# Optimization experiments

Hardware: AMD Instinct MI355X
Metric: run time of the kernel (lower is better)

The kernel has to match this reference:

```python
import jax, jax.numpy as jnp
import numpy as np

N_EMBD = 2048
HEAD_DIM = 128
N_CTX = 2048
BATCH = 8
SEQ = 2048


def setup_inputs() -> dict:
    key = jax.random.key(0)
    ks = jax.random.split(key, 7)
    s = 1.0 / np.sqrt(N_EMBD)
    x = jax.random.normal(ks[0], (BATCH, SEQ, N_EMBD), dtype=jnp.float32)
    # torch Linear params: weight (out, in), bias (out,)
    Wq = jax.random.uniform(ks[1], (HEAD_DIM, N_EMBD), jnp.float32, -s, s)
    bq = jax.random.uniform(ks[2], (HEAD_DIM,), jnp.float32, -s, s)
    Wk = jax.random.uniform(ks[3], (HEAD_DIM, N_EMBD), jnp.float32, -s, s)
    bk = jax.random.uniform(ks[4], (HEAD_DIM,), jnp.float32, -s, s)
    Wv = jax.random.uniform(ks[5], (HEAD_DIM, N_EMBD), jnp.float32, -s, s)
    bv = jax.random.uniform(ks[6], (HEAD_DIM,), jnp.float32, -s, s)
    return {"x": x, "Wq": Wq, "bq": bq, "Wk": Wk, "bk": bk, "Wv": Wv, "bv": bv}


def reference(x, Wq, bq, Wk, bk, Wv, bv):
    # projections: y = x @ W^T + b
    q = jnp.einsum('bse,de->bsd', x, Wq) + bq  # (B, S, D)
    k = jnp.einsum('bse,de->bsd', x, Wk) + bk
    v = jnp.einsum('bse,de->bsd', x, Wv) + bv
    seq = x.shape[1]
    scores = jnp.einsum('bqd,bkd->bqk', q, k)  # (B, S, S)
    # causal mask: strictly-upper-triangular positions set to -inf (before scaling, as in source)
    causal = jnp.triu(jnp.ones((seq, seq), dtype=bool), k=1)
    scores = jnp.where(causal[None, :, :], -jnp.inf, scores)
    # NOTE: source scales by sqrt(seq_size), not sqrt(head_dim)
    weight = jax.nn.softmax(scores / jnp.sqrt(jnp.float32(seq)), axis=-1)
    return jnp.einsum('bqk,bkd->bqd', weight, v)
```

## Files before the change

kernel.cpp:

```cpp
#include <hip/hip_runtime.h>
#include <cmath>

#define BATCH 8
#define SEQ   2048
#define NEMB  2048
#define HD    128
#define NROWS (BATCH * SEQ)

typedef __bf16 v8bf __attribute__((ext_vector_type(8)));
typedef float  f32x4 __attribute__((ext_vector_type(4)));

union U8 { v8bf v; __bf16 b[8]; unsigned short e[8]; };
union F4 { f32x4 v; float f[4]; };

__device__ inline void async16(void* lds, const void* g) {
  __builtin_amdgcn_global_load_lds(
      (const __attribute__((address_space(1))) unsigned int*)g,
      (__attribute__((address_space(3))) unsigned int*)lds, 16, 0, 0);
}

__device__ inline v8bf cvt8(float4 a, float4 b) {
  U8 u;
  u.b[0] = (__bf16)a.x; u.b[1] = (__bf16)a.y; u.b[2] = (__bf16)a.z; u.b[3] = (__bf16)a.w;
  u.b[4] = (__bf16)b.x; u.b[5] = (__bf16)b.y; u.b[6] = (__bf16)b.z; u.b[7] = (__bf16)b.w;
  return u.v;
}

__global__ __launch_bounds__(256) void wpack_kernel(
    const float* __restrict__ Wq, const float* __restrict__ Wk,
    const float* __restrict__ Wv, __bf16* __restrict__ out) {
  const int idx = blockIdx.x * 256 + threadIdx.x;
  const int lane = idx & 63;
  const int g = idx >> 6;
  const int fg = g & 7;
  const int tt = (g >> 3) & 31;
  const int wn = (g >> 8) & 1;
  const int p  = g >> 9;
  const int n = fg >> 1, kk = fg & 1;
  const int row = wn * 64 + n * 16 + (lane & 15);
  const int k   = tt * 64 + kk * 32 + (lane >> 4) * 8;
  const float* __restrict__ W = p == 0 ? Wq : p == 1 ? Wk : Wv;
  const float4* s = (const float4*)(W + (size_t)row * NEMB + k);
  float4 f0 = s[0], f1 = s[1];
  *(v8bf*)(out + (size_t)idx * 8) = cvt8(f0, f1);
}

__global__ __launch_bounds__(256, 3) void qkv_proj_kernel(
    const float* __restrict__ x, const __bf16* __restrict__ Wpack,
    const float* __restrict__ bq, const float* __restrict__ bk,
    const float* __restrict__ bv,
    __bf16* __restrict__ Qb, __bf16* __restrict__ Kb, __bf16* __restrict__ Vb)
{
  const int bid0 = blockIdx.x;
  const int bid = ((bid0 & 7) * 96) + (bid0 >> 3);
  const int mt = bid / 3;
  const int proj = bid % 3;
  const float* __restrict__ bias = proj == 0 ? bq : proj == 1 ? bk : bv;
  __bf16* __restrict__ Out = proj == 0 ? Qb : proj == 1 ? Kb : Vb;
  const int m0 = mt * 64;

  __shared__ float Asm[64 * 64];

  const int t = threadIdx.x, lane = t & 63, w = t >> 6;
  const int wm = w >> 1, wn = w & 1;
  const int hi = lane >> 4, lo = lane & 15;

  const float* pa[4];
  char* la[4];
#pragma unroll
  for (int i = 0; i < 4; ++i) {
    const int r = (w * 4 + i) * 4 + (lane >> 4);
    const int c = (lane & 15) ^ (r & 7);
    pa[i] = x + (size_t)(m0 + r) * NEMB + c * 4;
    la[i] = (char*)Asm + (w * 4 + i) * 1024;
  }

  const __bf16* bp = Wpack + (size_t)(proj * 2 + wn) * 131072 + lane * 8;

  f32x4 acc[2][4];
  const f32x4 fz = {0.f, 0.f, 0.f, 0.f};
#pragma unroll
  for (int m = 0; m < 2; ++m)
#pragma unroll
    for (int n = 0; n < 4; ++n) acc[m][n] = fz;

  v8bf B0[4][2], B1[4][2];
  auto LOADB = [&](v8bf (&B)[4][2], int tt) {
    const __bf16* p = bp + tt * 4096;
#pragma unroll
    for (int n = 0; n < 4; ++n)
#pragma unroll
      for (int kk = 0; kk < 2; ++kk)
        B[n][kk] = *(const v8bf*)(p + (n * 2 + kk) * 512);
  };
  auto STAGE_A = [&](int tt) {
    const int k0 = tt * 64;
#pragma unroll
    for (int i = 0; i < 4; ++i) async16(la[i], pa[i] + k0);
  };
  auto STEP = [&](v8bf (&B)[4][2]) {
#pragma unroll
    for (int kk = 0; kk < 2; ++kk) {
      v8bf a[2];
#pragma unroll
      for (int m = 0; m < 2; ++m) {
        const int r = wm * 32 + m * 16 + lo;
        const int s = kk * 8 + hi * 2;
        const char* rowp = (const char*)Asm + r * 256;
        F4 a0, a1;
        a0.v = *(const f32x4*)(rowp + (((s)     ^ (r & 7)) << 4));
        a1.v = *(const f32x4*)(rowp + (((s + 1) ^ (r & 7)) << 4));
        U8 u;
#pragma unroll
        for (int q = 0; q < 4; ++q) {
          u.b[q]     = (__bf16)a0.f[q];
          u.b[q + 4] = (__bf16)a1.f[q];
        }
        a[m] = u.v;
      }
#pragma unroll
      for (int m = 0; m < 2; ++m)
#pragma unroll
        for (int n = 0; n < 4; ++n)
          acc[m][n] = __builtin_amdgcn_mfma_f32_16x16x32_bf16(a[m], B[n][kk], acc[m][n], 0, 0, 0);
    }
  };

  const int NT = NEMB / 64;
  LOADB(B0, 0);
  for (int tt = 0; tt < NT; tt += 2) {
    __syncthreads();
    STAGE_A(tt);
    LOADB(B1, tt + 1);
    __syncthreads();
    STEP(B0);
    __syncthreads();
    STAGE_A(tt + 1);
    if (tt + 2 < NT) LOADB(B0, tt + 2);
    __syncthreads();
    STEP(B1);
  }

#pragma unroll
  for (int n = 0; n < 4; ++n) {
    const int col = wn * 64 + n * 16 + lo;
    const float bi = bias[col];
#pragma unroll
    for (int m = 0; m < 2; ++m) {
#pragma unroll
      for (int r = 0; r < 4; ++r) {
        const int row = m0 + wm * 32 + m * 16 + hi * 4 + r;
        Out[(size_t)row * HD + col] = (__bf16)(acc[m][n][r] + bi);
      }
    }
  }
}

__global__ __launch_bounds__(256) void attn_kernel(
    const __bf16* __restrict__ Qb, const __bf16* __restrict__ Kb,
    const __bf16* __restrict__ Vb, float* __restrict__ Opart,
    float* __restrict__ Ml)
{
  const int bid0 = blockIdx.x;
  const int bid = ((bid0 & 7) << 6) + (bid0 >> 3);
  const int b = bid >> 6;
  const int qs = bid & 63;
  const int qt = qs >> 1;
  const int s  = qs & 1;
  const int q0 = qt * 64;
  const int half = (qt + 2) >> 1;
  const int kv_beg = s ? half : 0;
  const int kv_end = s ? (qt + 1) : half;
  const int nst = kv_end - kv_beg;

  const int t = threadIdx.x, lane = t & 63, w = t >> 6;
  const int hi = lane >> 4, lo = lane & 15;

  __shared__ __bf16 Ksm[2][64 * 128];
  __shared__ __bf16 Vtsm[2][128 * 64];
  __shared__ __bf16 Psm[4][16 * 64];

  v8bf aQ[4];
  {
    const __bf16* qp = Qb + ((size_t)(b * SEQ + q0 + w * 16 + lo)) * HD + hi * 8;
#pragma unroll
    for (int kk = 0; kk < 4; ++kk) aQ[kk] = *(const v8bf*)(qp + kk * 32);
  }

  const __bf16* kga[4];
#pragma unroll
  for (int i = 0; i < 4; ++i) {
    const int r = (w * 4 + i) * 4 + (lane >> 4);
    const int c = (lane & 15) ^ (r & 7);
    kga[i] = Kb + ((size_t)(b * SEQ) + r) * HD + c * 8;
  }

  const int keyg = t >> 4, dg = t & 15;
  U8 vv[4];

  f32x4 accO[8];
  const f32x4 fz = {0.f, 0.f, 0.f, 0.f};
#pragma unroll
  for (int n = 0; n < 8; ++n) accO[n] = fz;
  float m_s[4], l_s[4];
#pragma unroll
  for (int r = 0; r < 4; ++r) { m_s[r] = -INFINITY; l_s[r] = 0.f; }

  const float scale = 0.022097086912079608f;

  if (nst > 0) {
    auto STAGE_K = [&](int kv, int buf) {
      const size_t off = (size_t)kv * 64 * HD;
      char* kb = (char*)&Ksm[buf][0];
#pragma unroll
      for (int i = 0; i < 4; ++i) async16(kb + (w * 4 + i) * 1024, kga[i] + off);
    };
    auto LOAD_V = [&](int kv) {
      const __bf16* vp = Vb + ((size_t)(b * SEQ + kv * 64 + keyg * 4)) * HD + dg * 8;
#pragma unroll
      for (int j = 0; j < 4; ++j) vv[j].v = *(const v8bf*)(vp + (size_t)j * HD);
    };
    auto WRITE_VT = [&](int buf) {
      char* vb2 = (char*)&Vtsm[buf][0];
#pragma unroll
      for (int dd = 0; dd < 8; ++dd) {
        const int d = (dd + dg) & 7;
        ushort4 pk = make_ushort4(vv[0].e[d], vv[1].e[d], vv[2].e[d], vv[3].e[d]);
        const int row = dg * 8 + d;
        *(ushort4*)(vb2 + row * 128 + ((keyg * 8) ^ ((row & 7) << 4))) = pk;
      }
    };

    STAGE_K(kv_beg, 0);
    LOAD_V(kv_beg);
    WRITE_VT(0);
    __syncthreads();

    for (int t2 = 0; t2 < nst; ++t2) {
      const int kv = kv_beg + t2;
      const int cur = t2 & 1;
      const bool more = (t2 + 1 < nst);
      if (more) { STAGE_K(kv + 1, cur ^ 1); LOAD_V(kv + 1); }

      f32x4 accS[4];
#pragma unroll
      for (int n = 0; n < 4; ++n) accS[n] = fz;
      const char* ksm = (const char*)&Ksm[cur][0];
#pragma unroll
      for (int kk = 0; kk < 4; ++kk) {
        const int cb = kk * 64 + hi * 16;
        v8bf bk[4];
#pragma unroll
        for (int n = 0; n < 4; ++n) {
          const int r = n * 16 + lo;
          bk[n] = *(const v8bf*)(ksm + r * 256 + (cb ^ ((r & 7) << 4)));
        }
#pragma unroll
        for (int n = 0; n < 4; ++n)
          accS[n] = __builtin_amdgcn_mfma_f32_16x16x32_bf16(aQ[kk], bk[n], accS[n], 0, 0, 0);
      }

      float sv[4][4];
      const bool diag = (kv == qt);
#pragma unroll
      for (int n = 0; n < 4; ++n)
#pragma unroll
        for (int r = 0; r < 4; ++r) {
          float v = accS[n][r] * scale;
          if (diag) {
            const int key = kv * 64 + n * 16 + lo;
            const int qr = q0 + w * 16 + hi * 4 + r;
            if (key > qr) v = -INFINITY;
          }
          sv[n][r] = v;
        }

      float mx[4];
#pragma unroll
      for (int r = 0; r < 4; ++r) {
        mx[r] = fmaxf(fmaxf(sv[0][r], sv[1][r]), fmaxf(sv[2][r], sv[3][r]));
#pragma unroll
        for (int off = 1; off < 16; off <<= 1)
          mx[r] = fmaxf(mx[r], __shfl_xor(mx[r], off));
      }
      float corr[4], p[4][4], rs[4];
#pragma unroll
      for (int r = 0; r < 4; ++r) {
        const float mnew = fmaxf(m_s[r], mx[r]);
        corr[r] = __expf(m_s[r] - mnew);
        m_s[r] = mnew;
        rs[r] = 0.f;
      }
#pragma unroll
      for (int n = 0; n < 4; ++n)
#pragma unroll
        for (int r = 0; r < 4; ++r) {
          p[n][r] = __expf(sv[n][r] - m_s[r]);
          rs[r] += p[n][r];
        }
#pragma unroll
      for (int r = 0; r < 4; ++r) {
#pragma unroll
        for (int off = 1; off < 16; off <<= 1) rs[r] += __shfl_xor(rs[r], off);
        l_s[r] = l_s[r] * corr[r] + rs[r];
      }
#pragma unroll
      for (int n = 0; n < 8; ++n)
#pragma unroll
        for (int r = 0; r < 4; ++r) accO[n][r] *= corr[r];

#pragma unroll
      for (int n = 0; n < 4; ++n)
#pragma unroll
        for (int r = 0; r < 4; ++r) {
          const int row = hi * 4 + r;
          __bf16 h = (__bf16)p[n][r];
          *(unsigned short*)((char*)&Psm[w][0] + row * 128 +
                             (((n * 16 + lo) * 2) ^ ((row & 7) << 4))) =
              __builtin_bit_cast(unsigned short, h);
        }

      if (more) WRITE_VT(cur ^ 1);

      const char* vsm = (const char*)&Vtsm[cur][0];
#pragma unroll
      for (int k2 = 0; k2 < 2; ++k2) {
        const int cb = k2 * 64 + hi * 16;
        const v8bf aP = *(const v8bf*)((const char*)&Psm[w][0] + lo * 128 + (cb ^ ((lo & 7) << 4)));
#pragma unroll
        for (int n = 0; n < 8; ++n) {
          const int r = n * 16 + lo;
          const v8bf bv = *(const v8bf*)(vsm + r * 128 + (cb ^ ((r & 7) << 4)));
          accO[n] = __builtin_amdgcn_mfma_f32_16x16x32_bf16(aP, bv, accO[n], 0, 0, 0);
        }
      }
      if (more) __syncthreads();
    }
  }

#pragma unroll
  for (int r = 0; r < 4; ++r) {
    const int qr = q0 + w * 16 + hi * 4 + r;
    float* op = Opart + ((size_t)s * NROWS + b * SEQ + qr) * HD + lo;
#pragma unroll
    for (int n = 0; n < 8; ++n) op[n * 16] = accO[n][r];
    if (lo == 0) {
      float* mlp = Ml + ((size_t)s * NROWS + b * SEQ + qr) * 2;
      mlp[0] = m_s[r];
      mlp[1] = l_s[r];
    }
  }
}

__global__ __launch_bounds__(256) void combine_kernel(
    const float* __restrict__ Opart, const float* __restrict__ Ml,
    float* __restrict__ out)
{
  const int idx = blockIdx.x * 256 + threadIdx.x;
  const int row = idx >> 1, h = idx & 1;
  const float m0 = Ml[(size_t)row * 2],           l0 = Ml[(size_t)row * 2 + 1];
  const float m1 = Ml[((size_t)NROWS + row) * 2], l1 = Ml[((size_t)NROWS + row) * 2 + 1];
  const float M = fmaxf(m0, m1);
  const float e0 = __expf(m0 - M), e1 = __expf(m1 - M);
  const float inv = 1.f / (l0 * e0 + l1 * e1);
  const float4* p0 = (const float4*)(Opart + (size_t)row * HD + h * 64);
  const float4* p1 = (const float4*)(Opart + ((size_t)NROWS + row) * HD + h * 64);
  float4* po = (float4*)(out + (size_t)row * HD + h * 64);
#pragma unroll
  for (int j = 0; j < 16; ++j) {
    float4 a = p0[j], c = p1[j];
    float4 r;
    r.x = (a.x * e0 + c.x * e1) * inv;
    r.y = (a.y * e0 + c.y * e1) * inv;
    r.z = (a.z * e0 + c.z * e1) * inv;
    r.w = (a.w * e0 + c.w * e1) * inv;
    po[j] = r;
  }
}

extern "C" void kernel_launch(void* const* d_in, const int* in_sizes, int n_in,
                              void* d_out, int out_size, void* d_ws, size_t ws_size,
                              hipStream_t stream) {
  const float* x  = (const float*)d_in[0];
  const float* Wq = (const float*)d_in[1];
  const float* bq = (const float*)d_in[2];
  const float* Wk = (const float*)d_in[3];
  const float* bk = (const float*)d_in[4];
  const float* Wv = (const float*)d_in[5];
  const float* bv = (const float*)d_in[6];
  float* out = (float*)d_out;

  __bf16* Qb = (__bf16*)d_ws;
  __bf16* Kb = Qb + (size_t)NROWS * HD;
  __bf16* Vb = Kb + (size_t)NROWS * HD;
  __bf16* Wpack = Vb + (size_t)NROWS * HD;
  float*  Opart = (float*)(Wpack + (size_t)3 * HD * NEMB);
  float*  Ml    = Opart + (size_t)2 * NROWS * HD;

  wpack_kernel<<<dim3(384), dim3(256), 0, stream>>>(Wq, Wk, Wv, Wpack);
  qkv_proj_kernel<<<dim3(256 * 3), dim3(256), 0, stream>>>(
      x, Wpack, bq, bk, bv, Qb, Kb, Vb);
  attn_kernel<<<dim3(BATCH * 32 * 2), dim3(256), 0, stream>>>(Qb, Kb, Vb, Opart, Ml);
  combine_kernel<<<dim3(NROWS * 2 / 256), dim3(256), 0, stream>>>(Opart, Ml, out);
}
```

Before: 131.4 us.

## Triple-buffer A tile in LDS with vmcnt-based waits in QKV projection

```diff
diff --git a/kernel.cpp b/kernel.cpp
--- a/kernel.cpp
+++ b/kernel.cpp
@@ -59,20 +59,20 @@
   __bf16* __restrict__ Out = proj == 0 ? Qb : proj == 1 ? Kb : Vb;
   const int m0 = mt * 64;
 
-  __shared__ float Asm[64 * 64];
+  __shared__ float Asm[3][64 * 64];
 
   const int t = threadIdx.x, lane = t & 63, w = t >> 6;
   const int wm = w >> 1, wn = w & 1;
   const int hi = lane >> 4, lo = lane & 15;
 
   const float* pa[4];
-  char* la[4];
+  int laOff[4];
 #pragma unroll
   for (int i = 0; i < 4; ++i) {
     const int r = (w * 4 + i) * 4 + (lane >> 4);
     const int c = (lane & 15) ^ (r & 7);
     pa[i] = x + (size_t)(m0 + r) * NEMB + c * 4;
-    la[i] = (char*)Asm + (w * 4 + i) * 1024;
+    laOff[i] = (w * 4 + i) * 1024;
   }
 
   const __bf16* bp = Wpack + (size_t)(proj * 2 + wn) * 131072 + lane * 8;
@@ -85,20 +85,22 @@
     for (int n = 0; n < 4; ++n) acc[m][n] = fz;
 
   v8bf B0[4][2], B1[4][2];
-  auto LOADB = [&](v8bf (&B)[4][2], int tt) {
-    const __bf16* p = bp + tt * 4096;
+  auto LOADB = [&](v8bf (&B)[4][2], int tt2) {
+    const __bf16* p = bp + tt2 * 4096;
 #pragma unroll
     for (int n = 0; n < 4; ++n)
 #pragma unroll
       for (int kk = 0; kk < 2; ++kk)
         B[n][kk] = *(const v8bf*)(p + (n * 2 + kk) * 512);
   };
-  auto STAGE_A = [&](int tt) {
-    const int k0 = tt * 64;
-#pragma unroll
-    for (int i = 0; i < 4; ++i) async16(la[i], pa[i] + k0);
+  auto STAGE_A = [&](int tt2, int buf) {
+    const int k0 = tt2 * 64;
+    char* base = (char*)&Asm[0][0] + buf * 16384;
+#pragma unroll
+    for (int i = 0; i < 4; ++i) async16(base + laOff[i], pa[i] + k0);
   };
-  auto STEP = [&](v8bf (&B)[4][2]) {
+  auto STEP = [&](int buf, v8bf (&B)[4][2]) {
+    const char* abase = (const char*)&Asm[0][0] + buf * 16384;
 #pragma unroll
     for (int kk = 0; kk < 2; ++kk) {
       v8bf a[2];
@@ -106,7 +108,7 @@
       for (int m = 0; m < 2; ++m) {
         const int r = wm * 32 + m * 16 + lo;
         const int s = kk * 8 + hi * 2;
-        const char* rowp = (const char*)Asm + r * 256;
+        const char* rowp = abase + r * 256;
         F4 a0, a1;
         a0.v = *(const f32x4*)(rowp + (((s)     ^ (r & 7)) << 4));
         a1.v = *(const f32x4*)(rowp + (((s + 1) ^ (r & 7)) << 4));
@@ -127,18 +129,30 @@
   };
 
   const int NT = NEMB / 64;
+  STAGE_A(0, 0);
   LOADB(B0, 0);
+  int rb = 0, wb = 1;
   for (int tt = 0; tt < NT; tt += 2) {
-    __syncthreads();
-    STAGE_A(tt);
-    LOADB(B1, tt + 1);
-    __syncthreads();
-    STEP(B0);
-    __syncthreads();
-    STAGE_A(tt + 1);
-    if (tt + 2 < NT) LOADB(B0, tt + 2);
-    __syncthreads();
-    STEP(B1);
+    {
+      STAGE_A(tt + 1, wb);
+      LOADB(B1, tt + 1);
+      asm volatile("s_waitcnt vmcnt(20)" ::: "memory");
+      __builtin_amdgcn_s_barrier();
+      STEP(rb, B0);
+      rb = wb; wb = (wb == 2) ? 0 : wb + 1;
+    }
+    {
+      if (tt + 2 < NT) {
+        STAGE_A(tt + 2, wb);
+        LOADB(B0, tt + 2);
+        asm volatile("s_waitcnt vmcnt(20)" ::: "memory");
+      } else {
+        asm volatile("s_waitcnt vmcnt(8)" ::: "memory");
+      }
+      __builtin_amdgcn_s_barrier();
+      STEP(rb, B1);
+      rb = wb; wb = (wb == 2) ? 0 : wb + 1;
+    }
   }
 
 #pragma unroll
```

Result: no change. 129.8 us (-1.2%).
